# Optimization experiments

Hardware: AMD Instinct MI355X
Metric: run time of the kernel (lower is better)

Reference implementation:

```python
import jax, jax.numpy as jnp
import numpy as np
import math

B, S, D = 16, 512, 512
H = 8
RET = 512  # return_dim, multiple of D
EPS = 1e-12


def _xavier(key, shape):
    bound = math.sqrt(6.0 / (shape[0] + shape[1]))
    return jax.random.uniform(key, shape, jnp.float32, -bound, bound)


def setup_inputs() -> dict:
    key = jax.random.key(0)
    ks = jax.random.split(key, 7)
    x = jax.random.normal(ks[0], (B, S, D), jnp.float32)
    WQ = _xavier(ks[1], (D, D))
    WK = _xavier(ks[2], (D, D))
    WV = _xavier(ks[3], (D, D))
    # LazyLinear over flattened (S*D) features; stored [in, out] for clean matmul
    Wlin = jax.random.normal(ks[4], (S * D, RET), jnp.float32) / math.sqrt(S * D)
    blin = jnp.zeros((RET,), jnp.float32)
    ln_w = jnp.ones((D,), jnp.float32)
    ln_b = jnp.zeros((D,), jnp.float32)
    return {"x": x, "WQ": WQ, "WK": WK, "WV": WV,
            "Wlin": Wlin, "blin": blin, "ln_w": ln_w, "ln_b": ln_b}


def _swish(v):
    return v * jax.nn.sigmoid(v)


def reference(x, WQ, WK, WV, Wlin, blin, ln_w, ln_b):
    b, s, d = x.shape
    dh = d // H
    # QKV projections -> [b, h, s, dh]
    Q = (x @ WQ).reshape(b, s, H, dh).transpose(0, 2, 1, 3)
    K = (x @ WK).reshape(b, s, H, dh).transpose(0, 2, 1, 3)
    V = (x @ WV).reshape(b, s, H, dh).transpose(0, 2, 1, 3)
    # swish-gated attention scores (no softmax)
    scores = jnp.einsum('bhqd,bhkd->bhqk', Q, K) / math.sqrt(dh)
    scores = _swish(scores)
    out = jnp.einsum('bhqk,bhkd->bqhd', scores, V).reshape(b, s, d)
    # residual + TF-style LayerNorm (residual_coef = 1)
    out = out + x
    u = out.mean(-1, keepdims=True)
    var = jnp.mean((out - u) ** 2, axis=-1, keepdims=True)
    out = ln_w * ((out - u) / jnp.sqrt(var + EPS)) + ln_b
    # linear over flattened seq*d features, swish, reshape (dropout = identity, eval)
    y = out.reshape(b, -1) @ Wlin + blin
    y = _swish(y)
    return y.reshape(b, -1, d)
```

## Files before the change

### kernel.cpp

```cpp
#include <hip/hip_runtime.h>
#include <cstdint>

#define TB 16
#define TS 512
#define TD 512
#define TH 8
#define TDH 64
#define TSD (TS*TD)

typedef __attribute__((ext_vector_type(8))) short s16x8;
typedef __attribute__((ext_vector_type(4))) float f32x4;
typedef unsigned short bfu;

__device__ __forceinline__ unsigned short f2b(float f) {
  unsigned int u = __float_as_uint(f);
  u += 0x7FFFu + ((u >> 16) & 1u);
  return (unsigned short)(u >> 16);
}
__device__ __forceinline__ float b2f(bfu h) {
  return __uint_as_float(((unsigned)h) << 16);
}

__device__ __forceinline__ void gll16(const void* g, void* l) {
  __builtin_amdgcn_global_load_lds((const __attribute__((address_space(1))) void*)g,
                                   (__attribute__((address_space(3))) void*)l, 16, 0, 0);
}

__device__ __forceinline__ f32x4 MFMA16(s16x8 a, s16x8 b, f32x4 c) {
  return __builtin_amdgcn_mfma_f32_16x16x32_bf16(a, b, c, 0, 0, 0);
}

__global__ __launch_bounds__(256) void k_prep(const float* __restrict__ x, ushort4* __restrict__ xb,
                                              const float* __restrict__ WQ, const float* __restrict__ WK,
                                              const float* __restrict__ WV, bfu* __restrict__ wt) {
  int t = threadIdx.x;
  if (blockIdx.x < 4096) {
    int i = blockIdx.x * 256 + t;
    float4 v = ((const float4*)x)[i];
    ushort4 o; o.x = f2b(v.x); o.y = f2b(v.y); o.z = f2b(v.z); o.w = f2b(v.w);
    xb[i] = o;
    return;
  }
  __shared__ float tile[64][65];
  int bid = blockIdx.x - 4096;
  int bk = bid & 7;
  int bn = bid >> 3;
  const float* W = bn < 8 ? WQ : (bn < 16 ? WK : WV);
  int ncol0 = (bn & 7) * 64;
  int tx = t & 63, ty = t >> 6;
  #pragma unroll
  for (int i = 0; i < 16; ++i) {
    int kl = i * 4 + ty;
    tile[kl][tx] = W[(size_t)(bk * 64 + kl) * 512 + ncol0 + tx];
  }
  __syncthreads();
  #pragma unroll
  for (int i = 0; i < 16; ++i) {
    int nl = i * 4 + ty;
    wt[(size_t)(bn * 64 + nl) * 512 + bk * 64 + tx] = f2b(tile[tx][nl]);
  }
}

__global__ __launch_bounds__(256) void k_qkv(const bfu* __restrict__ xb, const bfu* __restrict__ wt,
                                             bfu* __restrict__ qb, bfu* __restrict__ kb, bfu* __restrict__ vtb) {
  __shared__ __align__(16) bfu At[2][128 * 32];
  __shared__ __align__(16) bfu Bt[2][128 * 32];
  int t = threadIdx.x, lane = t & 63, w = t >> 6;
  int wr = w >> 1, wc = w & 1;
  int m0 = blockIdx.x * 128, n0 = blockIdx.y * 128;
  int fr = lane & 15, hi = lane >> 4;
  int l4r = lane >> 2, l4c = lane & 3;
  f32x4 acc[4][4] = {};

#define QKV_STAGE(BUF, K0) { \
    _Pragma("unroll") \
    for (int i = 0; i < 2; ++i) { \
      int row = i * 64 + w * 16 + l4r; \
      int cs = l4c ^ (l4r & 3);                         \
      gll16(xb + (size_t)(m0 + row) * TD + (K0) + cs * 8, (char*)At[BUF] + (i * 256 + w * 64) * 16); \
      gll16(wt + (size_t)(n0 + row) * TD + (K0) + cs * 8, (char*)Bt[BUF] + (i * 256 + w * 64) * 16); \
    } }

#define QKV_COMP(BUF) { \
    s16x8 a[4], bb[4]; \
    int ca = (hi ^ (fr & 3)) * 8; \
    _Pragma("unroll") \
    for (int m = 0; m < 4; ++m) a[m]  = *(const s16x8*)&At[BUF][(wr * 64 + m * 16 + fr) * 32 + ca]; \
    _Pragma("unroll") \
    for (int n = 0; n < 4; ++n) bb[n] = *(const s16x8*)&Bt[BUF][(wc * 64 + n * 16 + fr) * 32 + ca]; \
    _Pragma("unroll") \
    for (int m = 0; m < 4; ++m) \
      _Pragma("unroll") \
      for (int n = 0; n < 4; ++n) \
        acc[m][n] = MFMA16(a[m], bb[n], acc[m][n]); }

  QKV_STAGE(0, 0)
  __syncthreads();
  for (int k = 0; k < 16; ++k) {
    int cur = k & 1;
    if (k < 15) QKV_STAGE(cur ^ 1, (k + 1) * 32)
    QKV_COMP(cur)
    __syncthreads();
  }
#undef QKV_STAGE
#undef QKV_COMP

  #pragma unroll
  for (int m = 0; m < 4; ++m) {
    int grow = m0 + wr * 64 + m * 16 + hi * 4;
    #pragma unroll
    for (int n = 0; n < 4; ++n) {
      int gcol = n0 + wc * 64 + n * 16 + fr;
      if (gcol < 512) {
        #pragma unroll
        for (int r = 0; r < 4; ++r) qb[(size_t)(grow + r) * TD + gcol] = f2b(acc[m][n][r]);
      } else if (gcol < 1024) {
        int c = gcol - 512;
        #pragma unroll
        for (int r = 0; r < 4; ++r) kb[(size_t)(grow + r) * TD + c] = f2b(acc[m][n][r]);
      } else {
        int c = gcol - 1024;
        int hh = c >> 6, dc = c & 63;
        int b_ = grow >> 9, s = grow & 511;
        ushort4 pk;
        pk.x = f2b(acc[m][n][0]); pk.y = f2b(acc[m][n][1]);
        pk.z = f2b(acc[m][n][2]); pk.w = f2b(acc[m][n][3]);
        *(ushort4*)&vtb[((size_t)((b_ * TH + hh) * TDH + dc) << 9) + s] = pk;
      }
    }
  }
}

__global__ __launch_bounds__(256) void k_attn(const bfu* __restrict__ qb, const bfu* __restrict__ kb,
                                              const bfu* __restrict__ vtb, const bfu* __restrict__ xb,
                                              float* __restrict__ ao) {
  __shared__ __align__(16) bfu Qs[64 * 64];
  __shared__ __align__(16) bfu Ks[128 * 64];
  __shared__ __align__(16) bfu Vs[64 * 128];
  __shared__ __align__(16) bfu Ps[64 * 128];
  int t = threadIdx.x, lane = t & 63, w = t >> 6;
  int qt = blockIdx.x, h = blockIdx.y, b = blockIdx.z;
  size_t qrow0 = (size_t)b * TS + qt * 64;
  int fr = lane & 15, hi = lane >> 4;
  int l8r = lane >> 3, l8c = lane & 7;
  int l16r = lane >> 4, l16c = lane & 15;

#define K_STAGE(KT) { \
    _Pragma("unroll") \
    for (int i = 0; i < 4; ++i) { \
      int row = i * 32 + w * 8 + l8r; \
      int cs = l8c ^ (l8r & 7);                         \
      gll16(kb + ((size_t)b * TS + (KT) * 128 + row) * TD + h * TDH + cs * 8, \
            (char*)Ks + (i * 256 + w * 64) * 16); \
    } }
#define V_STAGE(KT) { \
    _Pragma("unroll") \
    for (int i = 0; i < 4; ++i) { \
      int row = i * 16 + w * 4 + l16r; \
      int cs = l16c ^ (row & 7); \
      gll16(vtb + ((size_t)(b * TH + h) * TDH + row) * TS + (KT) * 128 + cs * 8, \
            (char*)Vs + (i * 256 + w * 64) * 16); \
    } }

  #pragma unroll
  for (int i = 0; i < 2; ++i) {
    int row = i * 32 + w * 8 + l8r;
    int cs = l8c ^ (l8r & 7);
    gll16(qb + (qrow0 + row) * TD + h * TDH + cs * 8, (char*)Qs + (i * 256 + w * 64) * 16);
  }
  K_STAGE(0)
  V_STAGE(0)
  __syncthreads();

  int qrow = w * 16 + fr;
  int r7 = fr & 7;
  f32x4 acc_o[4] = {};
  for (int kt = 0; kt < 4; ++kt) {
    s16x8 aq0 = *(const s16x8*)&Qs[qrow * 64 + ((hi ^ r7) * 8)];
    s16x8 aq1 = *(const s16x8*)&Qs[qrow * 64 + (((4 + hi) ^ r7) * 8)];
    f32x4 sc[8];
    #pragma unroll
    for (int kj = 0; kj < 8; ++kj) {
      int krow = kj * 16 + fr;
      s16x8 b0 = *(const s16x8*)&Ks[krow * 64 + ((hi ^ r7) * 8)];
      s16x8 b1 = *(const s16x8*)&Ks[krow * 64 + (((4 + hi) ^ r7) * 8)];
      f32x4 c = {};
      c = MFMA16(aq0, b0, c);
      c = MFMA16(aq1, b1, c);
      sc[kj] = c;
    }
    #pragma unroll
    for (int kj = 0; kj < 8; ++kj) {
      #pragma unroll
      for (int r = 0; r < 4; ++r) {
        float v = sc[kj][r] * 0.125f;
        float p = v / (1.f + __expf(-v));
        int prow = w * 16 + hi * 4 + r;
        int c8 = (kj * 2 + (fr >> 3)) ^ (prow & 7);
        Ps[prow * 128 + c8 * 8 + (fr & 7)] = f2b(p);
      }
    }
    #pragma unroll
    for (int ks = 0; ks < 4; ++ks) {
      s16x8 pa = *(const s16x8*)&Ps[qrow * 128 + (((ks * 4 + hi) ^ r7) * 8)];
      #pragma unroll
      for (int dn = 0; dn < 4; ++dn) {
        s16x8 vb = *(const s16x8*)&Vs[(dn * 16 + fr) * 128 + (((ks * 4 + hi) ^ r7) * 8)];
        acc_o[dn] = MFMA16(pa, vb, acc_o[dn]);
      }
    }
    __syncthreads();
    if (kt < 3) {
      K_STAGE(kt + 1)
      V_STAGE(kt + 1)
      __syncthreads();
    }
  }
#undef K_STAGE
#undef V_STAGE
  #pragma unroll
  for (int dn = 0; dn < 4; ++dn) {
    int col = h * TDH + dn * 16 + fr;
    #pragma unroll
    for (int r = 0; r < 4; ++r) {
      size_t row = qrow0 + w * 16 + hi * 4 + r;
      ao[row * TD + col] = acc_o[dn][r] + b2f(xb[row * TD + col]);
    }
  }
}

__global__ __launch_bounds__(256) void k_ln(const float* __restrict__ a, const float* __restrict__ w,
                                            const float* __restrict__ bias, bfu* __restrict__ o) {
  int row = blockIdx.x, t = threadIdx.x;
  float2 v = *(const float2*)(a + (size_t)row * TD + t * 2);
  float s = v.x + v.y;
  #pragma unroll
  for (int off = 32; off > 0; off >>= 1) s += __shfl_down(s, off);
  __shared__ float r1[4], r2[4];
  int lane = t & 63, wv = t >> 6;
  if (lane == 0) r1[wv] = s;
  __syncthreads();
  float mean = (r1[0] + r1[1] + r1[2] + r1[3]) * (1.f / TD);
  float dx = v.x - mean, dy = v.y - mean;
  float q = dx * dx + dy * dy;
  #pragma unroll
  for (int off = 32; off > 0; off >>= 1) q += __shfl_down(q, off);
  if (lane == 0) r2[wv] = q;
  __syncthreads();
  float var = (r2[0] + r2[1] + r2[2] + r2[3]) * (1.f / TD);
  float inv = rsqrtf(var + 1e-12f);
  float2 wv2 = *(const float2*)(w + t * 2);
  float2 bv2 = *(const float2*)(bias + t * 2);
  unsigned pack = (unsigned)f2b(wv2.x * dx * inv + bv2.x) |
                  ((unsigned)f2b(wv2.y * dy * inv + bv2.y) << 16);
  *(unsigned*)(o + (size_t)row * TD + t * 2) = pack;
}

__global__ __launch_bounds__(256) void k_lin_mfma(const bfu* __restrict__ lno, const float* __restrict__ wl,
                                                  float* __restrict__ part) {
  __shared__ __align__(16) bfu Wt[64 * 72];
  int t = threadIdx.x, lane = t & 63, w = t >> 6;
  int fr = lane & 15, hi = lane >> 4;
  int kc = blockIdx.x >> 3, nb = blockIdx.x & 7;
  int n0 = nb * 64;
  int nl = t & 63, kb = (t >> 6) * 16;
  int ks0 = kc * 2048;
  const float* wbase = wl + (size_t)(ks0 + kb) * 512 + n0 + nl;
  const bfu*   abase = lno + (size_t)fr * TSD + ks0 + hi * 8;
  f32x4 acc = {};
  float wA[16], wB[16];
  s16x8 aA0, aA1, aB0, aB1;
  #pragma unroll
  for (int i = 0; i < 16; ++i) wA[i] = __builtin_nontemporal_load(wbase + (size_t)i * 512);
  aA0 = *(const s16x8*)abase;
  aA1 = *(const s16x8*)(abase + 32);

#define LIN_STEP(CW, CA0, CA1, NW, NA0, NA1, S)                                   \
  { if (S) __syncthreads();                                                       \
    unsigned pk[8];                                                               \
    _Pragma("unroll")                                                             \
    for (int i = 0; i < 8; ++i)                                                   \
      pk[i] = (unsigned)f2b(CW[2*i]) | ((unsigned)f2b(CW[2*i+1]) << 16);          \
    *(uint4*)&Wt[nl * 72 + kb]     = *(uint4*)&pk[0];                             \
    *(uint4*)&Wt[nl * 72 + kb + 8] = *(uint4*)&pk[4];                             \
    if ((S) + 1 < 32) {                                                           \
      const float* wp2 = wbase + (size_t)((S) + 1) * 64 * 512;                    \
      _Pragma("unroll")                                                           \
      for (int i = 0; i < 16; ++i) NW[i] = __builtin_nontemporal_load(wp2 + (size_t)i * 512); \
      const bfu* ap2 = abase + ((S) + 1) * 64;                                    \
      NA0 = *(const s16x8*)ap2; NA1 = *(const s16x8*)(ap2 + 32);                  \
    }                                                                             \
    __syncthreads();                                                              \
    s16x8 b0 = *(const s16x8*)&Wt[(w * 16 + fr) * 72 + hi * 8];                   \
    s16x8 b1 = *(const s16x8*)&Wt[(w * 16 + fr) * 72 + 32 + hi * 8];              \
    acc = MFMA16(CA0, b0, acc);                                                   \
    acc = MFMA16(CA1, b1, acc); }

  for (int s = 0; s < 32; s += 2) {
    LIN_STEP(wA, aA0, aA1, wB, aB0, aB1, s)
    LIN_STEP(wB, aB0, aB1, wA, aA0, aA1, s + 1)
  }
#undef LIN_STEP
  #pragma unroll
  for (int r = 0; r < 4; ++r)
    part[(size_t)kc * 8192 + (hi * 4 + r) * 512 + n0 + w * 16 + fr] = acc[r];
}

__global__ __launch_bounds__(256) void k_lin_red(const float* __restrict__ part, const float* __restrict__ blin,
                                                 float* __restrict__ out) {
  int o = blockIdx.x * 256 + threadIdx.x;
  float s = 0.f;
  #pragma unroll 16
  for (int c = 0; c < 128; ++c) s += part[(size_t)c * 8192 + o];
  float v = s + blin[o & 511];
  out[o] = v / (1.f + __expf(-v));
}

extern "C" void kernel_launch(void* const* d_in, const int* in_sizes, int n_in,
                              void* d_out, int out_size, void* d_ws, size_t ws_size,
                              hipStream_t stream) {
  const float* x   = (const float*)d_in[0];
  const float* WQ  = (const float*)d_in[1];
  const float* WK  = (const float*)d_in[2];
  const float* WV  = (const float*)d_in[3];
  const float* Wl  = (const float*)d_in[4];
  const float* bl  = (const float*)d_in[5];
  const float* lnw = (const float*)d_in[6];
  const float* lnb = (const float*)d_in[7];
  float* out = (float*)d_out;
  char* ws = (char*)d_ws;
  bfu* xb  = (bfu*)ws;
  bfu* wt  = xb + 4194304;
  bfu* qb  = wt + 786432;
  bfu* kb  = qb + 4194304;
  bfu* vtb = kb + 4194304;
  float* attn = (float*)(vtb + 4194304);
  bfu*   lno  = (bfu*)(attn + 4194304);
  float* part = (float*)(lno + 4194304);

  k_prep    <<<4288, 256, 0, stream>>>(x, (ushort4*)xb, WQ, WK, WV, wt);
  k_qkv     <<<dim3(64, 12), 256, 0, stream>>>(xb, wt, qb, kb, vtb);
  k_attn    <<<dim3(8, 8, 16), 256, 0, stream>>>(qb, kb, vtb, xb, attn);
  k_ln      <<<8192, 256, 0, stream>>>(attn, lnw, lnb, lno);
  k_lin_mfma<<<1024, 256, 0, stream>>>(lno, Wl, part);
  k_lin_red <<<32, 256, 0, stream>>>(part, bl, out);
}
```

Measured before the change: 185.7 us.

## Load Wlin straight into MFMA B fragments and use hardware bf16 pack conversion

```diff
diff --git a/kernel.cpp b/kernel.cpp
--- a/kernel.cpp
+++ b/kernel.cpp
@@ -12,10 +12,15 @@
 typedef __attribute__((ext_vector_type(4))) float f32x4;
 typedef unsigned short bfu;
 
+__device__ __forceinline__ unsigned cvt_pk(float lo, float hi) {
+  unsigned r;
+  asm("v_cvt_pk_bf16_f32 %0, %1, %2" : "=v"(r) : "v"(lo), "v"(hi));
+  return r;
+}
 __device__ __forceinline__ unsigned short f2b(float f) {
-  unsigned int u = __float_as_uint(f);
-  u += 0x7FFFu + ((u >> 16) & 1u);
-  return (unsigned short)(u >> 16);
+  unsigned r;
+  asm("v_cvt_pk_bf16_f32 %0, %1, %2" : "=v"(r) : "v"(f), "v"(f));
+  return (unsigned short)r;
 }
 __device__ __forceinline__ float b2f(bfu h) {
   return __uint_as_float(((unsigned)h) << 16);
@@ -30,14 +35,14 @@
   return __builtin_amdgcn_mfma_f32_16x16x32_bf16(a, b, c, 0, 0, 0);
 }
 
-__global__ __launch_bounds__(256) void k_prep(const float* __restrict__ x, ushort4* __restrict__ xb,
+__global__ __launch_bounds__(256) void k_prep(const float* __restrict__ x, uint2* __restrict__ xb,
                                               const float* __restrict__ WQ, const float* __restrict__ WK,
                                               const float* __restrict__ WV, bfu* __restrict__ wt) {
   int t = threadIdx.x;
   if (blockIdx.x < 4096) {
     int i = blockIdx.x * 256 + t;
     float4 v = ((const float4*)x)[i];
-    ushort4 o; o.x = f2b(v.x); o.y = f2b(v.y); o.z = f2b(v.z); o.w = f2b(v.w);
+    uint2 o; o.x = cvt_pk(v.x, v.y); o.y = cvt_pk(v.z, v.w);
     xb[i] = o;
     return;
   }
@@ -76,7 +81,7 @@
     _Pragma("unroll") \
     for (int i = 0; i < 2; ++i) { \
       int row = i * 64 + w * 16 + l4r; \
-      int cs = l4c ^ (l4r & 3);                         \
+      int cs = l4c ^ (l4r & 3); \
       gll16(xb + (size_t)(m0 + row) * TD + (K0) + cs * 8, (char*)At[BUF] + (i * 256 + w * 64) * 16); \
       gll16(wt + (size_t)(n0 + row) * TD + (K0) + cs * 8, (char*)Bt[BUF] + (i * 256 + w * 64) * 16); \
     } }
@@ -149,7 +154,7 @@
     _Pragma("unroll") \
     for (int i = 0; i < 4; ++i) { \
       int row = i * 32 + w * 8 + l8r; \
-      int cs = l8c ^ (l8r & 7);                         \
+      int cs = l8c ^ (l8r & 7); \
       gll16(kb + ((size_t)b * TS + (KT) * 128 + row) * TD + h * TDH + cs * 8, \
             (char*)Ks + (i * 256 + w * 64) * 16); \
     } }
@@ -251,59 +256,39 @@
   float inv = rsqrtf(var + 1e-12f);
   float2 wv2 = *(const float2*)(w + t * 2);
   float2 bv2 = *(const float2*)(bias + t * 2);
-  unsigned pack = (unsigned)f2b(wv2.x * dx * inv + bv2.x) |
-                  ((unsigned)f2b(wv2.y * dy * inv + bv2.y) << 16);
+  unsigned pack = cvt_pk(wv2.x * dx * inv + bv2.x, wv2.y * dy * inv + bv2.y);
   *(unsigned*)(o + (size_t)row * TD + t * 2) = pack;
 }
 
 __global__ __launch_bounds__(256) void k_lin_mfma(const bfu* __restrict__ lno, const float* __restrict__ wl,
                                                   float* __restrict__ part) {
-  __shared__ __align__(16) bfu Wt[64 * 72];
   int t = threadIdx.x, lane = t & 63, w = t >> 6;
   int fr = lane & 15, hi = lane >> 4;
   int kc = blockIdx.x >> 3, nb = blockIdx.x & 7;
-  int n0 = nb * 64;
-  int nl = t & 63, kb = (t >> 6) * 16;
+  int n0 = nb * 64 + w * 16;
   int ks0 = kc * 2048;
-  const float* wbase = wl + (size_t)(ks0 + kb) * 512 + n0 + nl;
+  const float* wbase = wl + (size_t)(ks0 + hi * 8) * 512 + n0 + fr;
   const bfu*   abase = lno + (size_t)fr * TSD + ks0 + hi * 8;
   f32x4 acc = {};
-  float wA[16], wB[16];
-  s16x8 aA0, aA1, aB0, aB1;
-  #pragma unroll
-  for (int i = 0; i < 16; ++i) wA[i] = __builtin_nontemporal_load(wbase + (size_t)i * 512);
-  aA0 = *(const s16x8*)abase;
-  aA1 = *(const s16x8*)(abase + 32);
-
-#define LIN_STEP(CW, CA0, CA1, NW, NA0, NA1, S)                                   \
-  { if (S) __syncthreads();                                                       \
-    unsigned pk[8];                                                               \
-    _Pragma("unroll")                                                             \
-    for (int i = 0; i < 8; ++i)                                                   \
-      pk[i] = (unsigned)f2b(CW[2*i]) | ((unsigned)f2b(CW[2*i+1]) << 16);          \
-    *(uint4*)&Wt[nl * 72 + kb]     = *(uint4*)&pk[0];                             \
-    *(uint4*)&Wt[nl * 72 + kb + 8] = *(uint4*)&pk[4];                             \
-    if ((S) + 1 < 32) {                                                           \
-      const float* wp2 = wbase + (size_t)((S) + 1) * 64 * 512;                    \
-      _Pragma("unroll")                                                           \
-      for (int i = 0; i < 16; ++i) NW[i] = __builtin_nontemporal_load(wp2 + (size_t)i * 512); \
-      const bfu* ap2 = abase + ((S) + 1) * 64;                                    \
-      NA0 = *(const s16x8*)ap2; NA1 = *(const s16x8*)(ap2 + 32);                  \
-    }                                                                             \
-    __syncthreads();                                                              \
-    s16x8 b0 = *(const s16x8*)&Wt[(w * 16 + fr) * 72 + hi * 8];                   \
-    s16x8 b1 = *(const s16x8*)&Wt[(w * 16 + fr) * 72 + 32 + hi * 8];              \
-    acc = MFMA16(CA0, b0, acc);                                                   \
-    acc = MFMA16(CA1, b1, acc); }
-
-  for (int s = 0; s < 32; s += 2) {
-    LIN_STEP(wA, aA0, aA1, wB, aB0, aB1, s)
-    LIN_STEP(wB, aB0, aB1, wA, aA0, aA1, s + 1)
-  }
-#undef LIN_STEP
+  #pragma unroll 2
+  for (int s = 0; s < 32; ++s) {
+    float wv[16];
+    #pragma unroll
+    for (int i = 0; i < 16; ++i)
+      wv[i] = __builtin_nontemporal_load(wbase + (size_t)(s * 64 + (i >> 3) * 32 + (i & 7)) * 512);
+    s16x8 a0 = *(const s16x8*)(abase + s * 64);
+    s16x8 a1 = *(const s16x8*)(abase + s * 64 + 32);
+    union { unsigned u[4]; s16x8 v; } b0, b1;
+    #pragma unroll
+    for (int i = 0; i < 4; ++i) b0.u[i] = cvt_pk(wv[2 * i], wv[2 * i + 1]);
+    #pragma unroll
+    for (int i = 0; i < 4; ++i) b1.u[i] = cvt_pk(wv[8 + 2 * i], wv[9 + 2 * i]);
+    acc = MFMA16(a0, b0.v, acc);
+    acc = MFMA16(a1, b1.v, acc);
+  }
   #pragma unroll
   for (int r = 0; r < 4; ++r)
-    part[(size_t)kc * 8192 + (hi * 4 + r) * 512 + n0 + w * 16 + fr] = acc[r];
+    part[(size_t)kc * 8192 + (hi * 4 + r) * 512 + n0 + fr] = acc[r];
 }
 
 __global__ __launch_bounds__(256) void k_lin_red(const float* __restrict__ part, const float* __restrict__ blin,
@@ -338,7 +323,7 @@
   bfu*   lno  = (bfu*)(attn + 4194304);
   float* part = (float*)(lno + 4194304);
 
-  k_prep    <<<4288, 256, 0, stream>>>(x, (ushort4*)xb, WQ, WK, WV, wt);
+  k_prep    <<<4288, 256, 0, stream>>>(x, (uint2*)xb, WQ, WK, WV, wt);
   k_qkv     <<<dim3(64, 12), 256, 0, stream>>>(xb, wt, qb, kb, vtb);
   k_attn    <<<dim3(8, 8, 16), 256, 0, stream>>>(qb, kb, vtb, xb, attn);
   k_ln      <<<8192, 256, 0, stream>>>(attn, lnw, lnb, lno);
```

Measured after the change: 231.2 us. +24.5%, slower.
